# Kernel tuning notes

Measured on AMD Instinct MI355X. Metric: run time of the kernel, lower is better.

The kernel has to match this reference:

```python
import jax, jax.numpy as jnp
import numpy as np

N_NODES = 100_000
N_EDGES = 1_000_000
D_X = 8
H = 128
N_DOM = 32768
N_BND = 8192
RE = 1.0 / 1.45e-05  # Reynolds number used in momentum residuals


def setup_inputs() -> dict:
    key = jax.random.key(0)
    ks = jax.random.split(key, 16)
    s = 0.05
    return {
        "x": jax.random.normal(ks[0], (N_NODES, D_X), jnp.float32),
        "x_mask": jax.random.uniform(ks[1], (N_NODES, 6), dtype=jnp.float32),
        "edge_index": jax.random.randint(ks[2], (2, N_EDGES), 0, N_NODES),
        "edge_attr": jax.random.normal(ks[3], (N_EDGES, 4), jnp.float32),
        "pos": jax.random.normal(ks[4], (N_NODES, 3), jnp.float32),
        "batch": jnp.zeros((N_NODES,), jnp.int32),
        "domain_sampling_points": jax.random.normal(ks[5], (N_DOM, 2), jnp.float32),
        "boundary_sampling_points": jax.random.normal(ks[6], (N_BND, 2), jnp.float32),
        "idxs_boundary_sampled": jax.random.randint(ks[7], (N_BND,), 0, N_NODES),
        # surrogate net parameters
        "Wx": jax.random.normal(ks[8], (D_X, H), jnp.float32) * s,
        "Wp": jax.random.normal(ks[9], (2, H), jnp.float32) * s,
        "We": jax.random.normal(ks[10], (3, H), jnp.float32) * s,
        "Wout": jax.random.normal(ks[11], (H, 3), jnp.float32) * s,
        "W1": jax.random.normal(ks[12], (2 + H, H), jnp.float32) * s,
        "b1": jnp.zeros((H,), jnp.float32),
        "W2": jax.random.normal(ks[13], (H, H), jnp.float32) * s,
        "b2": jnp.zeros((H,), jnp.float32),
        "W3": jax.random.normal(ks[14], (H, 3), jnp.float32) * s,
    }


def reference(x, x_mask, edge_index, edge_attr, pos, batch,
              domain_sampling_points, boundary_sampling_points,
              idxs_boundary_sampled,
              Wx, Wp, We, Wout, W1, b1, W2, b2, W3):
    pos2 = pos[:, :2]                              # pos = pos[:, :2]
    ea = edge_attr[:, jnp.array([0, 1, 3])]        # edge_attr[:, [0,1,3]]

    # --- surrogate GNN: one message-passing layer -> supervised output ---
    node_h = jnp.tanh(x @ Wx + pos2 @ Wp)          # [N, H]
    src, dst = edge_index[0], edge_index[1]
    msg = node_h[src] * (ea @ We)                  # [E, H] large gather (memory-bound)
    agg = jax.ops.segment_sum(msg, dst, num_segments=node_h.shape[0])
    h = jnp.tanh(node_h + agg)                     # [N, H]
    out_sup = h @ Wout                             # [N, 3]
    ctx = h.mean(axis=0)                           # [H] pooled graph context (constant wrt sp)

    # --- per-point coordinate network (u, v, p) ---
    def f_samp(sp):
        z = jnp.concatenate([sp, ctx])
        h1 = jnp.tanh(z @ W1 + b1)
        h2 = jnp.tanh(h1 @ W2 + b2)
        return h2 @ W3                             # [3] -> (u, v, p)

    sp = jnp.concatenate([domain_sampling_points, boundary_sampling_points])  # [S, 2]
    out_samp = jax.vmap(f_samp)(sp)                            # [S, 3]
    grads = jax.vmap(jax.jacrev(f_samp))(sp)                   # [S, 3, 2]
    hess = jax.vmap(jax.jacrev(jax.jacrev(f_samp)))(sp)        # [S, 3, 2, 2]

    nd = domain_sampling_points.shape[0]
    # --- domain (full_laminar) residuals ---
    u, v = out_samp[:nd, 0], out_samp[:nd, 1]
    u_x, u_y = grads[:nd, 0, 0], grads[:nd, 0, 1]
    v_x, v_y = grads[:nd, 1, 0], grads[:nd, 1, 1]
    p_x, p_y = grads[:nd, 2, 0], grads[:nd, 2, 1]
    u_xx, u_yy = hess[:nd, 0, 0, 0], hess[:nd, 0, 1, 1]
    v_xx, v_yy = hess[:nd, 1, 0, 0], hess[:nd, 1, 1, 1]
    continuity = u_x + v_y
    momentum_x = u * u_x + v * u_y + p_x - (u_xx + u_yy) / RE
    momentum_y = u * v_x + v * v_y + p_y - (v_xx + v_yy) / RE

    # --- boundary-condition residuals (vmapped BC math) ---
    bu, bv, bp = out_samp[nd:, 0], out_samp[nd:, 1], out_samp[nd:, 2]
    bu_x, bv_y = grads[nd:, 0, 0], grads[nd:, 1, 1]
    bp_x, bp_y = grads[nd:, 2, 0], grads[nd:, 2, 1]
    x_BC = x[idxs_boundary_sampled]                # [B, D_X]
    m = x_mask[idxs_boundary_sampled]              # [B, 6]
    t_x, t_y = x_BC[:, 0], x_BC[:, 1]
    n_x, n_y = -t_y, t_x
    r_vt = jnp.abs(t_x * bu + t_y * bv - x_BC[:, 2]) * m[:, 1]
    r_vn = jnp.abs(n_x * bu + n_y * bv - x_BC[:, 3]) * m[:, 2]
    r_p = jnp.abs(bp - x_BC[:, 4]) * m[:, 3]
    r_dvdn = jnp.abs(n_x * bu_x + n_y * bv_y - x_BC[:, 5]) * m[:, 4]
    r_dpdn = jnp.abs(n_x * bp_x + n_y * bp_y - x_BC[:, 6]) * m[:, 5]
    c = m[:, 1:6].sum(axis=1)
    boundary = (r_vt + r_vn + r_p + r_dvdn + r_dpdn) / c

    return (out_sup, continuity, momentum_x, momentum_y, boundary)
```

## Files before the change

### kernel.cpp

```cpp
#include <hip/hip_runtime.h>
#include <hip/hip_fp8.h>
#include <math.h>

#define H 128
#define DXI 8
#define NNODES 100000
#define NEDGES 1000000
#define NRUNS (NEDGES / 64)
#define NDOM 32768
#define NBND 8192
#define NPTS (NDOM + NBND)
#define INV_RE 1.45e-05f
#define NODE_BLOCKS 1024
#define NPR (NNODES / 8)

#define NSB ((NNODES + 1023) / 1024)

#define CONT_OFF (NNODES * 3)
#define MOMX_OFF (CONT_OFF + NDOM)
#define MOMY_OFF (MOMX_OFF + NDOM)
#define BND_OFF  (MOMY_OFF + NDOM)

#define KPAD 136
#define A_STRIDE (32 * KPAD)

typedef __attribute__((ext_vector_type(8))) short short8;
typedef __attribute__((ext_vector_type(4))) float f32x4;

__device__ __forceinline__ float fast_tanh(float x) {
    const float e = __builtin_amdgcn_exp2f(x * 2.88539008f);
    return fmaf(-2.f, __builtin_amdgcn_rcpf(e + 1.f), 1.f);
}

__device__ __forceinline__ unsigned pack_bf16(float a, float b) {
    unsigned ua = __float_as_uint(a), ub = __float_as_uint(b);
    ua += 0x7fffu + ((ua >> 16) & 1u);
    ub += 0x7fffu + ((ub >> 16) & 1u);
    return (ua >> 16) | (ub & 0xffff0000u);
}

__device__ __forceinline__ short to_bf16(float f) {
    unsigned u = __float_as_uint(f);
    u += 0x7fffu + ((u >> 16) & 1u);
    return (short)(u >> 16);
}

__global__ __launch_bounds__(256) void hist_th_kernel(
    const int* __restrict__ eidx, const float* __restrict__ x,
    const float* __restrict__ pos,
    const float* __restrict__ Wx, const float* __restrict__ Wp,
    int* __restrict__ counts, unsigned short* __restrict__ th,
    uint4* __restrict__ agg4)
{
    const int lane = threadIdx.x & 63;
    const int wv   = threadIdx.x >> 6;
    const int c0 = lane * 2, c1 = c0 + 1;

    const int gid = blockIdx.x * 256 + threadIdx.x;
    const uint4 z = make_uint4(0u, 0u, 0u, 0u);
    for (size_t i = gid; i < (size_t)NNODES * 16; i += (size_t)gridDim.x * 256)
        agg4[i] = z;

    float wxa[DXI], wxb_[DXI];
#pragma unroll
    for (int k = 0; k < DXI; ++k) { wxa[k] = Wx[k * H + c0]; wxb_[k] = Wx[k * H + c1]; }
    const float wp00 = Wp[c0], wp01 = Wp[H + c0];
    const float wp10 = Wp[c1], wp11 = Wp[H + c1];

    for (int n = blockIdx.x * 4 + wv; n < NNODES; n += gridDim.x * 4) {
        const float* xr = x + (size_t)n * DXI;
        const float px = pos[(size_t)n * 3], py = pos[(size_t)n * 3 + 1];
        float a0 = fmaf(wp00, px, wp01 * py);
        float a1 = fmaf(wp10, px, wp11 * py);
#pragma unroll
        for (int k = 0; k < DXI; ++k) {
            const float xv = xr[k];
            a0 = fmaf(xv, wxa[k], a0);
            a1 = fmaf(xv, wxb_[k], a1);
        }
        const __hip_fp8_e4m3 q0(fast_tanh(a0));
        const __hip_fp8_e4m3 q1(fast_tanh(a1));
        th[(size_t)n * 64 + lane] =
            (unsigned short)((unsigned)q0.__x | ((unsigned)q1.__x << 8));
    }

    const int* dst = eidx + NEDGES;
    const int G   = gridDim.x >> 3;
    const int g   = blockIdx.x >> 3;
    const int r   = blockIdx.x & 7;
    const int dlo = r * NPR, dhi = dlo + NPR;
    for (int e = g * 256 + threadIdx.x; e < NEDGES; e += G * 256) {
        const int d = dst[e];
        if (d >= dlo && d < dhi) atomicAdd(&counts[d], 1);
    }
}

__global__ __launch_bounds__(256) void scan1_kernel(
    const int* __restrict__ counts, int* __restrict__ excl, int* __restrict__ bsum)
{
    const int tid = threadIdx.x, b = blockIdx.x;
    const int base = b * 1024 + tid * 4;
    int v0 = 0, v1 = 0, v2 = 0, v3 = 0;
    if (base + 3 < NNODES) {
        const int4 t = *(const int4*)(counts + base);
        v0 = t.x; v1 = t.y; v2 = t.z; v3 = t.w;
    } else {
        if (base     < NNODES) v0 = counts[base];
        if (base + 1 < NNODES) v1 = counts[base + 1];
        if (base + 2 < NNODES) v2 = counts[base + 2];
        if (base + 3 < NNODES) v3 = counts[base + 3];
    }
    const int own = v0 + v1 + v2 + v3;
    int s = own;
    const int lane = tid & 63, wv = tid >> 6;
#pragma unroll
    for (int d = 1; d < 64; d <<= 1) {
        const int t = __shfl_up(s, d);
        if (lane >= d) s += t;
    }
    __shared__ int wsum[4];
    if (lane == 63) wsum[wv] = s;
    __syncthreads();
    int woff = 0;
    for (int w = 0; w < wv; ++w) woff += wsum[w];
    const int e0 = s - own + woff;
    const int e1 = e0 + v0, e2 = e1 + v1, e3 = e2 + v2;
    if (base + 3 < NNODES) {
        *(int4*)(excl + base) = make_int4(e0, e1, e2, e3);
    } else {
        if (base     < NNODES) excl[base]     = e0;
        if (base + 1 < NNODES) excl[base + 1] = e1;
        if (base + 2 < NNODES) excl[base + 2] = e2;
        if (base + 3 < NNODES) excl[base + 3] = e3;
    }
    if (tid == 0) bsum[b] = wsum[0] + wsum[1] + wsum[2] + wsum[3];
}

__global__ __launch_bounds__(128) void scan2_kernel(int* __restrict__ bsum)
{
    const int tid = threadIdx.x;
    int v = (tid < NSB) ? bsum[tid] : 0;
    const int own = v;
    const int lane = tid & 63, wv = tid >> 6;
#pragma unroll
    for (int d = 1; d < 64; d <<= 1) {
        const int t = __shfl_up(v, d);
        if (lane >= d) v += t;
    }
    __shared__ int ws2[2];
    if (lane == 63) ws2[wv] = v;
    __syncthreads();
    if (wv == 1) v += ws2[0];
    if (tid < NSB) bsum[tid] = v - own;
}

__global__ __launch_bounds__(256) void scan3_kernel(
    int* __restrict__ offsets, int* __restrict__ cursor, const int* __restrict__ bsum)
{
    const int tid = threadIdx.x, b = blockIdx.x;
    const int base = b * 1024 + tid * 4;
    const int add = bsum[b];
    if (base + 3 < NNODES) {
        int4 t = *(const int4*)(offsets + base);
        t.x += add; t.y += add; t.z += add; t.w += add;
        *(int4*)(offsets + base) = t;
        *(int4*)(cursor + base) = t;
    } else {
        for (int i = 0; i < 4; ++i)
            if (base + i < NNODES) {
                const int t = offsets[base + i] + add;
                offsets[base + i] = t;
                cursor[base + i] = t;
            }
    }
}

__global__ __launch_bounds__(256) void scatter_kernel(
    const int* __restrict__ eidx, const float* __restrict__ eattr,
    int* __restrict__ cursor, uint4* __restrict__ csrE)
{
    const int* dst = eidx + NEDGES;
    const int G   = gridDim.x >> 3;
    const int g   = blockIdx.x >> 3;
    const int r   = blockIdx.x & 7;
    const int dlo = r * NPR, dhi = dlo + NPR;
    for (int e = g * 256 + threadIdx.x; e < NEDGES; e += G * 256) {
        const int d = dst[e];
        if (d >= dlo && d < dhi) {
            const float4 ea = ((const float4*)eattr)[e];
            const int slot = atomicAdd(&cursor[d], 1);
            uint4 rec;
            rec.x = (unsigned)eidx[e];
            rec.y = (unsigned)d;
            rec.z = pack_bf16(ea.x, ea.y);
            rec.w = pack_bf16(ea.w, 0.f);
            csrE[slot] = rec;
        }
    }
}

__global__ __launch_bounds__(256) void seg_edge_kernel(
    const uint4* __restrict__ csrE, const unsigned short* __restrict__ th,
    const float* __restrict__ We, unsigned* __restrict__ agg)
{
    const int run = blockIdx.x * 4 + (threadIdx.x >> 6);
    if (run >= NRUNS) return;
    const int lane = threadIdx.x & 63;
    const int c0 = lane * 2, c1 = c0 + 1;

    const float wea0 = We[c0], wea1 = We[H + c0], wea2 = We[2 * H + c0];
    const float web0 = We[c1], web1 = We[H + c1], web2 = We[2 * H + c1];

    const uint4 rec = csrE[(size_t)run * 64 + lane];
    const int mydst = (int)rec.y;

    float acc0 = 0.f, acc1 = 0.f;
    bool first = true;
    int cur = __builtin_amdgcn_readlane(mydst, 0);

#pragma unroll
    for (int sub = 0; sub < 4; ++sub) {
        unsigned short rowv[16];
#pragma unroll
        for (int t = 0; t < 16; ++t) {
            const int s = __builtin_amdgcn_readlane((int)rec.x, sub * 16 + t);
            rowv[t] = th[(size_t)s * 64 + lane];
        }
#pragma unroll
        for (int t = 0; t < 16; ++t) {
            const int e = sub * 16 + t;
            const unsigned ue01 = (unsigned)__builtin_amdgcn_readlane((int)rec.z, e);
            const unsigned ue3  = (unsigned)__builtin_amdgcn_readlane((int)rec.w, e);
            const float e0f = __uint_as_float(ue01 << 16);
            const float e1f = __uint_as_float(ue01 & 0xffff0000u);
            const float e3f = __uint_as_float(ue3 << 16);
            __hip_fp8_e4m3 d0, d1;
            d0.__x = (__hip_fp8_storage_t)(rowv[t] & 0xff);
            d1.__x = (__hip_fp8_storage_t)(rowv[t] >> 8);
            const float th0 = (float)d0;
            const float th1 = (float)d1;
            const float w0 = fmaf(e0f, wea0, fmaf(e1f, wea1, e3f * wea2));
            const float w1 = fmaf(e0f, web0, fmaf(e1f, web1, e3f * web2));
            acc0 = fmaf(th0, w0, acc0);
            acc1 = fmaf(th1, w1, acc1);

            const int nxt = (e < 63) ? __builtin_amdgcn_readlane(mydst, e + 1) : -1;
            if (nxt != cur) {
                unsigned* p = agg + (size_t)cur * 64 + lane;
                if (first || e == 63) {
                    unsigned old = *p;
                    while (true) {
                        const float g0 = __uint_as_float(old << 16) + acc0;
                        const float g1 = __uint_as_float(old & 0xffff0000u) + acc1;
                        const unsigned nw = pack_bf16(g0, g1);
                        const unsigned prev = atomicCAS(p, old, nw);
                        if (prev == old) break;
                        old = prev;
                    }
                } else {
                    *p = pack_bf16(acc0, acc1);
                }
                acc0 = 0.f; acc1 = 0.f;
                first = false;
                cur = nxt;
            }
        }
    }
}

__global__ __launch_bounds__(256) void node_kernel(
    const float* __restrict__ x, const float* __restrict__ pos,
    const unsigned* __restrict__ agg,
    const float* __restrict__ Wx, const float* __restrict__ Wp,
    const float* __restrict__ Wout,
    float* __restrict__ out_sup, float* __restrict__ ctx_part)
{
    const int lane = threadIdx.x & 63;
    const int wv   = threadIdx.x >> 6;
    const int c0 = lane * 2, c1 = c0 + 1;

    float wxa[DXI], wxb_[DXI];
#pragma unroll
    for (int k = 0; k < DXI; ++k) { wxa[k] = Wx[k * H + c0]; wxb_[k] = Wx[k * H + c1]; }
    const float wp00 = Wp[c0], wp01 = Wp[H + c0];
    const float wp10 = Wp[c1], wp11 = Wp[H + c1];
    const float woa0 = Wout[c0 * 3], woa1 = Wout[c0 * 3 + 1], woa2 = Wout[c0 * 3 + 2];
    const float wob0 = Wout[c1 * 3], wob1 = Wout[c1 * 3 + 1], wob2 = Wout[c1 * 3 + 2];

    float ctx0 = 0.f, ctx1 = 0.f;

    for (int n = blockIdx.x * 4 + wv; n < NNODES; n += gridDim.x * 4) {
        const unsigned ag = agg[(size_t)n * 64 + lane];
        const float* xr = x + (size_t)n * DXI;
        const float px = pos[(size_t)n * 3], py = pos[(size_t)n * 3 + 1];
        float a0 = fmaf(wp00, px, wp01 * py);
        float a1 = fmaf(wp10, px, wp11 * py);
#pragma unroll
        for (int k = 0; k < DXI; ++k) {
            const float xv = xr[k];
            a0 = fmaf(xv, wxa[k], a0);
            a1 = fmaf(xv, wxb_[k], a1);
        }
        const float h0 = fast_tanh(fast_tanh(a0) + __uint_as_float(ag << 16));
        const float h1 = fast_tanh(fast_tanh(a1) + __uint_as_float(ag & 0xffff0000u));
        ctx0 += h0; ctx1 += h1;

        float p0 = fmaf(h0, woa0, h1 * wob0);
        float p1 = fmaf(h0, woa1, h1 * wob1);
        float p2 = fmaf(h0, woa2, h1 * wob2);
#pragma unroll
        for (int m = 32; m; m >>= 1) {
            p0 += __shfl_xor(p0, m);
            p1 += __shfl_xor(p1, m);
            p2 += __shfl_xor(p2, m);
        }
        if (lane == 0) {
            out_sup[(size_t)n * 3 + 0] = p0;
            out_sup[(size_t)n * 3 + 1] = p1;
            out_sup[(size_t)n * 3 + 2] = p2;
        }
    }

    __shared__ float part[4][H];
    part[wv][c0] = ctx0;
    part[wv][c1] = ctx1;
    __syncthreads();
    if (threadIdx.x < H) {
        const int ch = threadIdx.x;
        ctx_part[(size_t)blockIdx.x * H + ch] =
            part[0][ch] + part[1][ch] + part[2][ch] + part[3][ch];
    }
}

__global__ __launch_bounds__(128) void ctx_kernel(
    const float* __restrict__ ctx_part, const float* __restrict__ W1,
    const float* __restrict__ b1, float* __restrict__ tab)
{
    __shared__ float ctx[H];
    const int ch = threadIdx.x;
    float s0 = 0.f, s1 = 0.f, s2 = 0.f, s3 = 0.f;
#pragma unroll 4
    for (int b = 0; b < NODE_BLOCKS; b += 4) {
        s0 += ctx_part[(size_t)(b + 0) * H + ch];
        s1 += ctx_part[(size_t)(b + 1) * H + ch];
        s2 += ctx_part[(size_t)(b + 2) * H + ch];
        s3 += ctx_part[(size_t)(b + 3) * H + ch];
    }
    ctx[ch] = (s0 + s1 + s2 + s3) * (1.0f / (float)NNODES);
    __syncthreads();
    float acc = b1[ch];
    for (int k = 0; k < H; ++k) acc = fmaf(ctx[k], W1[(size_t)(2 + k) * H + ch], acc);
    const float A0 = W1[ch], A1 = W1[H + ch];
    tab[ch * 8 + 0] = A0;
    tab[ch * 8 + 1] = A1;
    tab[ch * 8 + 2] = acc;
    tab[ch * 8 + 3] = A0 * A0;
    tab[ch * 8 + 4] = A1 * A1;
    tab[ch * 8 + 5] = 0.f;
    tab[ch * 8 + 6] = 0.f;
    tab[ch * 8 + 7] = 0.f;
}

__global__ __launch_bounds__(256, 2) void samp_mfma_kernel(
    const float* __restrict__ dom, const float* __restrict__ bnd,
    const int* __restrict__ bidx,
    const float* __restrict__ x, const float* __restrict__ xmask,
    const float* __restrict__ tab,
    const float* __restrict__ W2, const float* __restrict__ b2,
    const float* __restrict__ W3, float* __restrict__ out)
{
    __shared__ __attribute__((aligned(16))) short Bt[128 * KPAD];
    __shared__ __attribute__((aligned(16))) short Alds[5 * A_STRIDE];
    __shared__ __attribute__((aligned(16))) float red[32][13];

    const int tid = threadIdx.x;
    const int blk = blockIdx.x;

    for (int i = tid; i < H * H; i += 256) {
        const int k = i >> 7, n = i & 127;
        Bt[n * KPAD + k] = to_bf16(W2[i]);
    }

    for (int idx = tid; idx < 32 * 64; idx += 256) {
        const int pl = idx >> 6;
        const int k0 = (idx & 63) * 2;
        const int p  = blk * 32 + pl;
        float spx, spy;
        if (p < NDOM) { spx = dom[(size_t)p * 2];          spy = dom[(size_t)p * 2 + 1]; }
        else          { spx = bnd[(size_t)(p - NDOM) * 2]; spy = bnd[(size_t)(p - NDOM) * 2 + 1]; }
        float v[2][5];
#pragma unroll
        for (int kk = 0; kk < 2; ++kk) {
            const int k = k0 + kk;
            const float4 t4 = *(const float4*)(tab + (size_t)k * 8);
            const float A1s = tab[(size_t)k * 8 + 4];
            const float A0 = t4.x, A1 = t4.y, cc = t4.z, A0s = t4.w;
            const float a1 = fmaf(spx, A0, fmaf(spy, A1, cc));
            const float e  = __builtin_amdgcn_exp2f(a1 * 2.88539008f);
            const float h1 = fmaf(-2.f, __builtin_amdgcn_rcpf(e + 1.f), 1.f);
            const float t1 = fmaf(-h1, h1, 1.f);
            const float m2 = -2.f * h1 * t1;
            v[kk][0] = h1;
            v[kk][1] = t1 * A0;
            v[kk][2] = t1 * A1;
            v[kk][3] = m2 * A0s;
            v[kk][4] = m2 * A1s;
        }
        const int base = pl * KPAD + k0;
#pragma unroll
        for (int q = 0; q < 5; ++q)
            *(unsigned*)&Alds[q * A_STRIDE + base] = pack_bf16(v[0][q], v[1][q]);
    }
    __syncthreads();

    const int lane = tid & 63;
    const int wv = tid >> 6;
    const int pt = wv >> 1;
    const int jh = wv & 1;
    const int ln = lane & 15;
    const int hi = lane >> 4;

    f32x4 acc[4][5];
#pragma unroll
    for (int nt = 0; nt < 4; ++nt)
#pragma unroll
        for (int q = 0; q < 5; ++q)
            acc[nt][q] = (f32x4){0.f, 0.f, 0.f, 0.f};

#pragma unroll
    for (int kc = 0; kc < 4; ++kc) {
        short8 af[5];
#pragma unroll
        for (int q = 0; q < 5; ++q)
            af[q] = *(const short8*)&Alds[q * A_STRIDE + (pt * 16 + ln) * KPAD + kc * 32 + hi * 8];
        short8 bfr[4];
#pragma unroll
        for (int nt = 0; nt < 4; ++nt)
            bfr[nt] = *(const short8*)&Bt[(jh * 64 + nt * 16 + ln) * KPAD + kc * 32 + hi * 8];
#pragma unroll
        for (int nt = 0; nt < 4; ++nt)
#pragma unroll
            for (int q = 0; q < 5; ++q)
                acc[nt][q] = __builtin_amdgcn_mfma_f32_16x16x32_bf16(af[q], bfr[nt], acc[nt][q], 0, 0, 0);
    }

    float w30[4], w31[4], w32[4], b2j[4];
#pragma unroll
    for (int nt = 0; nt < 4; ++nt) {
        const int j = jh * 64 + nt * 16 + ln;
        w30[nt] = W3[j * 3];
        w31[nt] = W3[j * 3 + 1];
        w32[nt] = W3[j * 3 + 2];
        b2j[nt] = b2[j];
    }

    float rr[4][13];
#pragma unroll
    for (int i = 0; i < 4; ++i)
#pragma unroll
        for (int c = 0; c < 13; ++c) rr[i][c] = 0.f;

#pragma unroll
    for (int i = 0; i < 4; ++i) {
#pragma unroll
        for (int nt = 0; nt < 4; ++nt) {
            const float a2v  = acc[nt][0][i] + b2j[nt];
            const float d2xv = acc[nt][1][i];
            const float d2yv = acc[nt][2][i];
            const float exxv = acc[nt][3][i];
            const float eyyv = acc[nt][4][i];
            const float h2 = fast_tanh(a2v);
            const float t2 = fmaf(-h2, h2, 1.f);
            const float gx = t2 * d2xv;
            const float gy = t2 * d2yv;
            const float hxx = fmaf(-2.f * h2 * gx, d2xv, t2 * exxv);
            const float hyy = fmaf(-2.f * h2 * gy, d2yv, t2 * eyyv);
            rr[i][0]  = fmaf(h2, w30[nt], rr[i][0]);
            rr[i][1]  = fmaf(h2, w31[nt], rr[i][1]);
            rr[i][2]  = fmaf(h2, w32[nt], rr[i][2]);
            rr[i][3]  = fmaf(gx, w30[nt], rr[i][3]);
            rr[i][4]  = fmaf(gx, w31[nt], rr[i][4]);
            rr[i][5]  = fmaf(gx, w32[nt], rr[i][5]);
            rr[i][6]  = fmaf(gy, w30[nt], rr[i][6]);
            rr[i][7]  = fmaf(gy, w31[nt], rr[i][7]);
            rr[i][8]  = fmaf(gy, w32[nt], rr[i][8]);
            rr[i][9]  = fmaf(hxx, w30[nt], rr[i][9]);
            rr[i][10] = fmaf(hxx, w31[nt], rr[i][10]);
            rr[i][11] = fmaf(hyy, w30[nt], rr[i][11]);
            rr[i][12] = fmaf(hyy, w31[nt], rr[i][12]);
        }
    }

#pragma unroll
    for (int m = 1; m < 16; m <<= 1)
#pragma unroll
        for (int i = 0; i < 4; ++i)
#pragma unroll
            for (int c = 0; c < 13; ++c)
                rr[i][c] += __shfl_xor(rr[i][c], m);

    if (ln == 0 && jh == 0) {
#pragma unroll
        for (int i = 0; i < 4; ++i) {
            const int pl = pt * 16 + hi * 4 + i;
#pragma unroll
            for (int c = 0; c < 13; ++c) red[pl][c] = rr[i][c];
        }
    }
    __syncthreads();
    if (ln == 0 && jh == 1) {
#pragma unroll
        for (int i = 0; i < 4; ++i) {
            const int pl = pt * 16 + hi * 4 + i;
#pragma unroll
            for (int c = 0; c < 13; ++c) red[pl][c] += rr[i][c];
        }
    }
    __syncthreads();

    if (tid < 32) {
        const int p = blk * 32 + tid;
        float s[13];
#pragma unroll
        for (int c = 0; c < 13; ++c) s[c] = red[tid][c];
        const float u = s[0], v = s[1], pp = s[2];
        const float ux = s[3], vx = s[4], px = s[5];
        const float uy = s[6], vy = s[7], py = s[8];
        const float uxx = s[9], vxx = s[10], uyy = s[11], vyy = s[12];
        if (p < NDOM) {
            out[CONT_OFF + p] = ux + vy;
            out[MOMX_OFF + p] = fmaf(u, ux, fmaf(v, uy, px)) - (uxx + uyy) * INV_RE;
            out[MOMY_OFF + p] = fmaf(u, vx, fmaf(v, vy, py)) - (vxx + vyy) * INV_RE;
        } else {
            const int i = p - NDOM;
            const int idx = bidx[i];
            const float* xbp = x + (size_t)idx * DXI;
            const float* mm = xmask + (size_t)idx * 6;
            const float tx = xbp[0], ty = xbp[1];
            const float nx = -ty, ny = tx;
            const float r_vt = fabsf(tx * u + ty * v - xbp[2]) * mm[1];
            const float r_vn = fabsf(nx * u + ny * v - xbp[3]) * mm[2];
            const float r_p  = fabsf(pp - xbp[4]) * mm[3];
            const float r_dv = fabsf(nx * ux + ny * vy - xbp[5]) * mm[4];
            const float r_dp = fabsf(nx * px + ny * py - xbp[6]) * mm[5];
            const float c = mm[1] + mm[2] + mm[3] + mm[4] + mm[5];
            out[BND_OFF + i] = (r_vt + r_vn + r_p + r_dv + r_dp) / c;
        }
    }
}

extern "C" void kernel_launch(void* const* d_in, const int* in_sizes, int n_in,
                              void* d_out, int out_size, void* d_ws, size_t ws_size,
                              hipStream_t stream) {
    const float* x     = (const float*)d_in[0];
    const float* xmask = (const float*)d_in[1];
    const int*   eidx  = (const int*)d_in[2];
    const float* eattr = (const float*)d_in[3];
    const float* pos   = (const float*)d_in[4];
    const float* dom   = (const float*)d_in[6];
    const float* bnd   = (const float*)d_in[7];
    const int*   bidx  = (const int*)d_in[8];
    const float* Wx    = (const float*)d_in[9];
    const float* Wp    = (const float*)d_in[10];
    const float* We    = (const float*)d_in[11];
    const float* Wout  = (const float*)d_in[12];
    const float* W1    = (const float*)d_in[13];
    const float* b1    = (const float*)d_in[14];
    const float* W2    = (const float*)d_in[15];
    const float* b2    = (const float*)d_in[16];
    const float* W3    = (const float*)d_in[17];

    float* out = (float*)d_out;

    int*            counts   = (int*)d_ws;
    int*            offsets  = counts + NNODES;
    int*            cursor   = offsets + NNODES + 8;
    int*            bsum     = cursor + NNODES;
    uint4*          csrE     = (uint4*)(bsum + 128);
    unsigned short* th       = (unsigned short*)(csrE + NEDGES);
    unsigned*       agg      = (unsigned*)(th + (size_t)NNODES * 64);
    float*          ctx_part = (float*)(agg + (size_t)NNODES * 64);
    float*          tab      = ctx_part + (size_t)NODE_BLOCKS * H;

    (void)hipMemsetAsync(counts, 0, (size_t)NNODES * sizeof(int), stream);

    hist_th_kernel<<<2048, 256, 0, stream>>>(eidx, x, pos, Wx, Wp, counts, th, (uint4*)agg);
    scan1_kernel<<<NSB, 256, 0, stream>>>(counts, offsets, bsum);
    scan2_kernel<<<1, 128, 0, stream>>>(bsum);
    scan3_kernel<<<NSB, 256, 0, stream>>>(offsets, cursor, bsum);
    scatter_kernel<<<4096, 256, 0, stream>>>(eidx, eattr, cursor, csrE);
    seg_edge_kernel<<<(NRUNS + 3) / 4, 256, 0, stream>>>(csrE, th, We, agg);
    node_kernel<<<NODE_BLOCKS, 256, 0, stream>>>(x, pos, agg, Wx, Wp, Wout, out, ctx_part);
    ctx_kernel<<<1, H, 0, stream>>>(ctx_part, W1, b1, tab);
    samp_mfma_kernel<<<NPTS / 32, 256, 0, stream>>>(dom, bnd, bidx, x, xmask, tab, W2, b2, W3, out);
}
```

Before: 250.3 us.

## Split histogram into its own kernel and fuse node tanh/zeroing into scan1

Result: slower. 255.9 us (+2.3%).

```diff
diff --git a/kernel.cpp b/kernel.cpp
--- a/kernel.cpp
+++ b/kernel.cpp
@@ -45,22 +45,69 @@
     return (short)(u >> 16);
 }
 
-__global__ __launch_bounds__(256) void hist_th_kernel(
-    const int* __restrict__ eidx, const float* __restrict__ x,
-    const float* __restrict__ pos,
+__global__ __launch_bounds__(256) void hist_kernel(
+    const int* __restrict__ eidx, int* __restrict__ counts)
+{
+    const int* dst = eidx + NEDGES;
+    for (int e = blockIdx.x * 256 + threadIdx.x; e < NEDGES; e += gridDim.x * 256)
+        atomicAdd(&counts[dst[e]], 1);
+}
+
+__global__ __launch_bounds__(256) void scan1_kernel(
+    const int* __restrict__ counts, int* __restrict__ excl, int* __restrict__ bsum,
+    const float* __restrict__ x, const float* __restrict__ pos,
     const float* __restrict__ Wx, const float* __restrict__ Wp,
-    int* __restrict__ counts, unsigned short* __restrict__ th,
-    uint4* __restrict__ agg4)
-{
-    const int lane = threadIdx.x & 63;
-    const int wv   = threadIdx.x >> 6;
-    const int c0 = lane * 2, c1 = c0 + 1;
-
-    const int gid = blockIdx.x * 256 + threadIdx.x;
+    unsigned short* __restrict__ th, uint4* __restrict__ agg4)
+{
+    const int tid = threadIdx.x;
+
+    if (blockIdx.x < NSB) {
+        const int b = blockIdx.x;
+        const int base = b * 1024 + tid * 4;
+        int v0 = 0, v1 = 0, v2 = 0, v3 = 0;
+        if (base + 3 < NNODES) {
+            const int4 t = *(const int4*)(counts + base);
+            v0 = t.x; v1 = t.y; v2 = t.z; v3 = t.w;
+        } else {
+            if (base     < NNODES) v0 = counts[base];
+            if (base + 1 < NNODES) v1 = counts[base + 1];
+            if (base + 2 < NNODES) v2 = counts[base + 2];
+            if (base + 3 < NNODES) v3 = counts[base + 3];
+        }
+        const int own = v0 + v1 + v2 + v3;
+        int s = own;
+        const int lane = tid & 63, wv = tid >> 6;
+#pragma unroll
+        for (int d = 1; d < 64; d <<= 1) {
+            const int t = __shfl_up(s, d);
+            if (lane >= d) s += t;
+        }
+        __shared__ int wsum[4];
+        if (lane == 63) wsum[wv] = s;
+        __syncthreads();
+        int woff = 0;
+        for (int w = 0; w < wv; ++w) woff += wsum[w];
+        const int e0 = s - own + woff;
+        const int e1 = e0 + v0, e2 = e1 + v1, e3 = e2 + v2;
+        if (base + 3 < NNODES) {
+            *(int4*)(excl + base) = make_int4(e0, e1, e2, e3);
+        } else {
+            if (base     < NNODES) excl[base]     = e0;
+            if (base + 1 < NNODES) excl[base + 1] = e1;
+            if (base + 2 < NNODES) excl[base + 2] = e2;
+            if (base + 3 < NNODES) excl[base + 3] = e3;
+        }
+        if (tid == 0) bsum[b] = wsum[0] + wsum[1] + wsum[2] + wsum[3];
+    }
+
+    const int gid = blockIdx.x * 256 + tid;
     const uint4 z = make_uint4(0u, 0u, 0u, 0u);
     for (size_t i = gid; i < (size_t)NNODES * 16; i += (size_t)gridDim.x * 256)
         agg4[i] = z;
 
+    const int lane = tid & 63;
+    const int wv   = tid >> 6;
+    const int c0 = lane * 2, c1 = c0 + 1;
     float wxa[DXI], wxb_[DXI];
 #pragma unroll
     for (int k = 0; k < DXI; ++k) { wxa[k] = Wx[k * H + c0]; wxb_[k] = Wx[k * H + c1]; }
@@ -83,57 +130,6 @@
         th[(size_t)n * 64 + lane] =
             (unsigned short)((unsigned)q0.__x | ((unsigned)q1.__x << 8));
     }
-
-    const int* dst = eidx + NEDGES;
-    const int G   = gridDim.x >> 3;
-    const int g   = blockIdx.x >> 3;
-    const int r   = blockIdx.x & 7;
-    const int dlo = r * NPR, dhi = dlo + NPR;
-    for (int e = g * 256 + threadIdx.x; e < NEDGES; e += G * 256) {
-        const int d = dst[e];
-        if (d >= dlo && d < dhi) atomicAdd(&counts[d], 1);
-    }
-}
-
-__global__ __launch_bounds__(256) void scan1_kernel(
-    const int* __restrict__ counts, int* __restrict__ excl, int* __restrict__ bsum)
-{
-    const int tid = threadIdx.x, b = blockIdx.x;
-    const int base = b * 1024 + tid * 4;
-    int v0 = 0, v1 = 0, v2 = 0, v3 = 0;
-    if (base + 3 < NNODES) {
-        const int4 t = *(const int4*)(counts + base);
-        v0 = t.x; v1 = t.y; v2 = t.z; v3 = t.w;
-    } else {
-        if (base     < NNODES) v0 = counts[base];
-        if (base + 1 < NNODES) v1 = counts[base + 1];
-        if (base + 2 < NNODES) v2 = counts[base + 2];
-        if (base + 3 < NNODES) v3 = counts[base + 3];
-    }
-    const int own = v0 + v1 + v2 + v3;
-    int s = own;
-    const int lane = tid & 63, wv = tid >> 6;
-#pragma unroll
-    for (int d = 1; d < 64; d <<= 1) {
-        const int t = __shfl_up(s, d);
-        if (lane >= d) s += t;
-    }
-    __shared__ int wsum[4];
-    if (lane == 63) wsum[wv] = s;
-    __syncthreads();
-    int woff = 0;
-    for (int w = 0; w < wv; ++w) woff += wsum[w];
-    const int e0 = s - own + woff;
-    const int e1 = e0 + v0, e2 = e1 + v1, e3 = e2 + v2;
-    if (base + 3 < NNODES) {
-        *(int4*)(excl + base) = make_int4(e0, e1, e2, e3);
-    } else {
-        if (base     < NNODES) excl[base]     = e0;
-        if (base + 1 < NNODES) excl[base + 1] = e1;
-        if (base + 2 < NNODES) excl[base + 2] = e2;
-        if (base + 3 < NNODES) excl[base + 3] = e3;
-    }
-    if (tid == 0) bsum[b] = wsum[0] + wsum[1] + wsum[2] + wsum[3];
 }
 
 __global__ __launch_bounds__(128) void scan2_kernel(int* __restrict__ bsum)
@@ -584,8 +580,8 @@
 
     (void)hipMemsetAsync(counts, 0, (size_t)NNODES * sizeof(int), stream);
 
-    hist_th_kernel<<<2048, 256, 0, stream>>>(eidx, x, pos, Wx, Wp, counts, th, (uint4*)agg);
-    scan1_kernel<<<NSB, 256, 0, stream>>>(counts, offsets, bsum);
+    hist_kernel<<<1024, 256, 0, stream>>>(eidx, counts);
+    scan1_kernel<<<2048, 256, 0, stream>>>(counts, offsets, bsum, x, pos, Wx, Wp, th, (uint4*)agg);
     scan2_kernel<<<1, 128, 0, stream>>>(bsum);
     scan3_kernel<<<NSB, 256, 0, stream>>>(offsets, cursor, bsum);
     scatter_kernel<<<4096, 256, 0, stream>>>(eidx, eattr, cursor, csrE);
```
